# Optimization experiments

Hardware: AMD Instinct MI355X
Metric: run time of the kernel (lower is better)

## Reference

```python
import jax, jax.numpy as jnp
import numpy as np

B, S, D, H = 2, 2048, 4096, 32
Dh = D // H          # 128, rotary_dim == head_dim
BASE = 10000.0       # rope_theta
SCALE = Dh ** -0.5


def setup_inputs() -> dict:
    key = jax.random.key(0)
    k0, k1, k2 = jax.random.split(key, 3)
    w_scale = 0.02
    return {
        "hidden_states": jax.random.normal(k0, (B, S, D), jnp.float32),
        "positions": jnp.broadcast_to(jnp.arange(S, dtype=jnp.int32), (B, S)),
        "Wqkv": jax.random.normal(k1, (D, 3 * D), jnp.float32) * w_scale,
        "bqkv": jnp.zeros((3 * D,), jnp.float32),
        "Wproj": jax.random.normal(k2, (D, D), jnp.float32) * w_scale,
    }


def _apply_rope(x, positions):
    # x: [B, S, H, Dh]; neox-style (rotate-half) RoPE, as in vLLM PagedAttentionWithRoPE
    half = Dh // 2
    inv_freq = 1.0 / (BASE ** (jnp.arange(half, dtype=jnp.float32) / half))
    ang = positions[..., None].astype(jnp.float32) * inv_freq      # [B, S, half]
    cos = jnp.cos(ang)[:, :, None, :]                              # [B, S, 1, half]
    sin = jnp.sin(ang)[:, :, None, :]
    x1, x2 = x[..., :half], x[..., half:]
    return jnp.concatenate([x1 * cos - x2 * sin, x2 * cos + x1 * sin], axis=-1)


def reference(hidden_states, positions, Wqkv, bqkv, Wproj):
    # c_attn: fused QKV projection
    qkv = hidden_states @ Wqkv + bqkv                              # [B, S, 3D]
    q, k, v = jnp.split(qkv, 3, axis=-1)
    q = q.reshape(B, S, H, Dh)
    k = k.reshape(B, S, H, Dh)
    v = v.reshape(B, S, H, Dh)
    # fused RoPE on q and k at the given positions
    q = _apply_rope(q, positions)
    k = _apply_rope(k, positions)
    # causal scaled-dot-product attention (prefill semantics of paged attention)
    scores = jnp.einsum("bqhd,bkhd->bhqk", q, k) * SCALE           # [B, H, S, S]
    causal = jnp.tril(jnp.ones((S, S), dtype=bool))
    scores = jnp.where(causal, scores, jnp.finfo(scores.dtype).min)
    attn = jax.nn.softmax(scores, axis=-1)
    ctx = jnp.einsum("bhqk,bkhd->bqhd", attn, v).reshape(B, S, D)
    # c_proj (no bias)
    return ctx @ Wproj
```

## Files before the change

### kernel.cpp

```cpp
#include <hip/hip_runtime.h>

typedef __attribute__((ext_vector_type(8))) short short8;
typedef __attribute__((ext_vector_type(4))) short short4v;
typedef __attribute__((ext_vector_type(4))) float f32x4;

#define LDS8(base, off) (*(const short8*)((const char*)(base) + (off)))
#define GLOAD_LDS16(gp, lp) __builtin_amdgcn_global_load_lds( \
    (const __attribute__((address_space(1))) unsigned int*)(gp), \
    (__attribute__((address_space(3))) unsigned int*)(lp), 16, 0, 0)
#define SBAR() __builtin_amdgcn_s_barrier()
#define WAIT_LGKM0() do { asm volatile("s_waitcnt lgkmcnt(0)"); __builtin_amdgcn_sched_barrier(0); } while (0)

__device__ __forceinline__ short f2bf(float f) {
    unsigned u = __builtin_bit_cast(unsigned, f);
    unsigned r = (u + 0x7FFFu + ((u >> 16) & 1u)) >> 16;
    return (short)r;
}
__device__ __forceinline__ float bf2f(short s) {
    unsigned u = ((unsigned)(unsigned short)s) << 16;
    return __builtin_bit_cast(float, u);
}

__global__ __launch_bounds__(256) void cvt_f32_bf16(const float* __restrict__ in,
                                                    short* __restrict__ out, int n8) {
    int i = blockIdx.x * 256 + threadIdx.x;
    if (i < n8) {
        const f32x4* p = (const f32x4*)(in + (size_t)i * 8);
        f32x4 a = p[0], bq = p[1];
        short8 o;
        o[0] = f2bf(a[0]); o[1] = f2bf(a[1]); o[2] = f2bf(a[2]); o[3] = f2bf(a[3]);
        o[4] = f2bf(bq[0]); o[5] = f2bf(bq[1]); o[6] = f2bf(bq[2]); o[7] = f2bf(bq[3]);
        *(short8*)(out + (size_t)i * 8) = o;
    }
}

__global__ __launch_bounds__(256) void transpose_cvt(const float* __restrict__ W,
                                                     short* __restrict__ Out, int R, int C) {
    __shared__ float tile[64][33];
    int c0 = blockIdx.x * 64, r0 = blockIdx.y * 32;
    int tid = threadIdx.x;
    int cc4 = (tid & 15) * 4;
#pragma unroll
    for (int it = 0; it < 2; ++it) {
        int rr = (tid >> 4) + it * 16;
        f32x4 v = *(const f32x4*)&W[(size_t)(r0 + rr) * C + c0 + cc4];
#pragma unroll
        for (int i = 0; i < 4; ++i) tile[cc4 + i][rr] = v[i];
    }
    __syncthreads();
    int cc = tid >> 2, r8 = (tid & 3) * 8;
    short8 o;
#pragma unroll
    for (int i = 0; i < 8; ++i) o[i] = f2bf(tile[cc][r8 + i]);
    *(short8*)&Out[(size_t)(c0 + cc) * R + r0 + r8] = o;
}

__global__ __launch_bounds__(256) void rope_table(float* __restrict__ ctab, float* __restrict__ stab) {
    int idx = blockIdx.x * 256 + threadIdx.x;
    int t = idx >> 6, j = idx & 63;
    float inv = expf(-(float)j * (9.210340371976184f / 64.0f));
    float ang = (float)t * inv;
    ctab[idx] = cosf(ang);
    stab[idx] = sinf(ang);
}

__global__ __launch_bounds__(256) void rope_scatter(const short* __restrict__ qkv,
                                                    const int* __restrict__ pos,
                                                    const float* __restrict__ ctab,
                                                    const float* __restrict__ stab,
                                                    short* __restrict__ Q, short* __restrict__ K) {
    int id = blockIdx.x * 256 + threadIdx.x;
    int j = id & 63;
    int h = (id >> 6) & 31;
    int s = (id >> 11) & 2047;
    int b = id >> 22;
    size_t qrow = (size_t)(b * 2048 + s) * 12288 + h * 128;
    float q1 = bf2f(qkv[qrow + j]),        q2 = bf2f(qkv[qrow + 64 + j]);
    float k1 = bf2f(qkv[qrow + 4096 + j]), k2 = bf2f(qkv[qrow + 4160 + j]);
    int p = pos[b * 2048 + s];
    float c = ctab[p * 64 + j], si = stab[p * 64 + j];
    size_t orow = ((size_t)(b * 32 + h) * 2048 + s) * 128;
    Q[orow + j]      = f2bf(q1 * c - q2 * si);
    Q[orow + 64 + j] = f2bf(q2 * c + q1 * si);
    K[orow + j]      = f2bf(k1 * c - k2 * si);
    K[orow + 64 + j] = f2bf(k2 * c + k1 * si);
}

__global__ __launch_bounds__(256) void v_transpose(const short* __restrict__ qkv,
                                                   short* __restrict__ Vt) {
    int bh = blockIdx.z; int b = bh >> 5, h = bh & 31;
    int s0 = blockIdx.x * 64, d0 = blockIdx.y * 64;
    __shared__ short tile[64][65];
    int tid = threadIdx.x;
    int sl = tid >> 3;
    int d8 = (tid & 7) * 8;
#pragma unroll
    for (int it = 0; it < 2; ++it) {
        int s = sl + it * 32;
        short8 v = *(const short8*)&qkv[(size_t)(b * 2048 + s0 + s) * 12288 + 8192 + h * 128 + d0 + d8];
#pragma unroll
        for (int i = 0; i < 8; ++i) tile[s][d8 + i] = v[i];
    }
    __syncthreads();
    int dl = tid >> 3;
    int s8 = (tid & 7) * 8;
#pragma unroll
    for (int it = 0; it < 2; ++it) {
        int d = dl + it * 32;
        short8 o;
#pragma unroll
        for (int i = 0; i < 8; ++i) o[i] = tile[s8 + i][d];
        *(short8*)&Vt[((size_t)bh * 128 + d0 + d) * 2048 + s0 + s8] = o;
    }
}

__global__ __launch_bounds__(512, 2) void gemm256(const short* __restrict__ A,
                                                  const short* __restrict__ Bt,
                                                  const float* __restrict__ bias,
                                                  short* __restrict__ Cbf,
                                                  float* __restrict__ Cf,
                                                  int M, int N, int K, int nN) {
    __shared__ __align__(16) char smem[131072];
    const int tid = threadIdx.x;
    const int l = tid & 63, w = tid >> 6;
    const int m = l & 15, g = l >> 4, m7 = m & 7;
    const int wm = w >> 2, wn = w & 3;

    int cpx = gridDim.x >> 3;
    int wg = (blockIdx.x & 7) * cpx + (blockIdx.x >> 3);
    int gsz = nN << 3;
    int grp = wg / gsz, rem = wg - grp * gsz;
    int bm = (grp << 3) + (rem & 7);
    int bn = rem >> 3;
    int m0 = bm << 8, n0 = bn << 8;

    const int srow = l >> 3;
    const int sgcol = ((l & 7) ^ srow) << 3;

    const int NT = K >> 6;

    const int AbaseR = wm << 14;
    const int BbaseR = 32768 + ((wn >> 1) << 14);
    const int brow0 = (wn & 1) << 6;

    f32x4 acc[8][4];
    const f32x4 fz = {0.f, 0.f, 0.f, 0.f};
#pragma unroll
    for (int i = 0; i < 8; ++i)
#pragma unroll
        for (int j = 0; j < 4; ++j) acc[i][j] = fz;

    auto stage_half = [&](const short* G, int grow0, int kcol, int ldsoff) {
        GLOAD_LDS16(G + (size_t)(grow0 +      w * 8 + srow) * K + kcol + sgcol,
                    smem + ldsoff + w * 1024);
        GLOAD_LDS16(G + (size_t)(grow0 + 64 + w * 8 + srow) * K + kcol + sgcol,
                    smem + ldsoff + 8192 + w * 1024);
    };

    short8 af[2][2], bf[4][2];

#define RD_A(I0)                                                                 \
    _Pragma("unroll")                                                            \
    for (int i2 = 0; i2 < 2; ++i2) {                                             \
        _Pragma("unroll")                                                        \
        for (int kk = 0; kk < 2; ++kk)                                           \
            af[i2][kk] = LDS8(Ab, (((I0) + i2) * 16 + m) * 128 + (((kk * 4 + g) ^ m7) << 4)); \
    }

#define MFMA_IP(IP)                                                              \
    do {                                                                         \
        __builtin_amdgcn_s_setprio(1);                                           \
        _Pragma("unroll")                                                        \
        for (int kk = 0; kk < 2; ++kk) {                                         \
            _Pragma("unroll")                                                    \
            for (int i2 = 0; i2 < 2; ++i2) {                                     \
                _Pragma("unroll")                                                \
                for (int j2 = 0; j2 < 4; ++j2) {                                 \
                    acc[(IP) * 2 + i2][j2] = __builtin_amdgcn_mfma_f32_16x16x32_bf16( \
                        af[i2][kk], bf[j2][kk], acc[(IP) * 2 + i2][j2], 0, 0, 0); \
                }                                                                \
            }                                                                    \
        }                                                                        \
        __builtin_amdgcn_s_setprio(0);                                           \
    } while (0)

#pragma unroll
    for (int t = 0; t < 2; ++t) {
        int sb = t << 16;
        stage_half(A,  m0,       t * 64, sb);
        stage_half(A,  m0 + 128, t * 64, sb + 16384);
        stage_half(Bt, n0,       t * 64, sb + 32768);
        stage_half(Bt, n0 + 128, t * 64, sb + 49152);
    }
    asm volatile("s_waitcnt vmcnt(8)");
    __builtin_amdgcn_sched_barrier(0);
    SBAR();

    for (int kt = 0; kt < NT; ++kt) {
        const int slotb = (kt & 1) << 16;
        const char* Ab = smem + slotb + AbaseR;
        const char* Bb = smem + slotb + BbaseR;
        const bool pf = (kt + 2) < NT;
        const int kc = (kt + 2) << 6;

#pragma unroll
        for (int j = 0; j < 4; ++j) {
#pragma unroll
            for (int kk = 0; kk < 2; ++kk)
                bf[j][kk] = LDS8(Bb, (brow0 + j * 16 + m) * 128 + (((kk * 4 + g) ^ m7) << 4));
        }
        RD_A(0);
        asm volatile("s_waitcnt lgkmcnt(8)");
        SBAR();
        WAIT_LGKM0();
        MFMA_IP(0);
        SBAR();

        RD_A(2);
        if (pf) stage_half(Bt, n0, kc, slotb + 32768);
        SBAR();
        WAIT_LGKM0();
        MFMA_IP(1);
        SBAR();

        RD_A(4);
        if (pf) stage_half(Bt, n0 + 128, kc, slotb + 49152);
        SBAR();
        WAIT_LGKM0();
        MFMA_IP(2);
        SBAR();

        RD_A(6);
        SBAR();
        WAIT_LGKM0();
        MFMA_IP(3);
        if (pf) {
            stage_half(A, m0,       kc, slotb);
            stage_half(A, m0 + 128, kc, slotb + 16384);
        }
        if (kt == NT - 2)     asm volatile("s_waitcnt vmcnt(0)");
        else if (kt < NT - 1) asm volatile("s_waitcnt vmcnt(6)");
        SBAR();
    }
#undef RD_A
#undef MFMA_IP

#pragma unroll
    for (int i = 0; i < 8; ++i) {
#pragma unroll
        for (int j = 0; j < 4; ++j) {
#pragma unroll
            for (int r = 0; r < 4; ++r) {
                int row = m0 + wm * 128 + i * 16 + g * 4 + r;
                int col = n0 + wn * 64 + j * 16 + m;
                float v = acc[i][j][r];
                if (bias) v += bias[col];
                if (Cbf) Cbf[(size_t)row * N + col] = f2bf(v);
                else     Cf[(size_t)row * N + col] = v;
            }
        }
    }
}

__global__ __launch_bounds__(512, 4) void flash_fwd(const short* __restrict__ Q,
                                                    const short* __restrict__ Kt,
                                                    const short* __restrict__ Vt,
                                                    short* __restrict__ ctx) {
    const int S = 2048;
    const float SCALE = 0.08838834764831845f;
    __shared__ __align__(16) char smem[81920];

    int tid = threadIdx.x, l = tid & 63, w = tid >> 6;
    int m = l & 15, g = l >> 4, m7 = m & 7;
    int qg = blockIdx.x, h = blockIdx.y, b = blockIdx.z;
    int bh = b * 32 + h;
    int q0 = qg * 128 + w * 16;

    const short* Qg = Q + ((size_t)bh * S + q0) * 128;
    const short* Kg = Kt + (size_t)bh * S * 128;
    const short* Vg = Vt + (size_t)bh * 128 * S;

    short8 qf[4];
#pragma unroll
    for (int kb = 0; kb < 4; ++kb)
        qf[kb] = *(const short8*)(Qg + m * 128 + kb * 32 + g * 8);

    const f32x4 fz = {0.f, 0.f, 0.f, 0.f};
    f32x4 O[8];
#pragma unroll
    for (int nb = 0; nb < 8; ++nb) O[nb] = fz;
    float Mr[4], Lr[4];
#pragma unroll
    for (int r = 0; r < 4; ++r) { Mr[r] = -__builtin_inff(); Lr[r] = 0.f; }

    const short* Kp[2]; const short* Vp[2]; int KlO[2], VlO[2];
#pragma unroll
    for (int q = 0; q < 2; ++q) {
        int c = w * 2 + q;
        int rowK = c * 4 + (l >> 4);
        Kp[q] = Kg + (size_t)rowK * 128 + (((l & 15) ^ (rowK & 7)) * 8);
        KlO[q] = c * 1024;
        int rowV = c * 8 + (l >> 3);
        Vp[q] = Vg + (size_t)rowV * S + (((l & 7) ^ (rowV & 7)) * 8);
        VlO[q] = c * 1024;
    }

    auto stage = [&](int t, int slot) {
#pragma unroll
        for (int q = 0; q < 2; ++q) {
            GLOAD_LDS16(Kp[q] + (size_t)t * 8192, smem + slot * 16384 + KlO[q]);
            GLOAD_LDS16(Vp[q] + t * 64, smem + 32768 + slot * 16384 + VlO[q]);
        }
    };

    int nkt = 2 * qg + 2;
    stage(0, 0);
    asm volatile("s_waitcnt vmcnt(0)");
    __builtin_amdgcn_sched_barrier(0);
    SBAR();

    for (int kt = 0; kt < nkt; ++kt) {
        if (kt + 1 < nkt) stage(kt + 1, (kt + 1) & 1);
        const char* Kl = smem + (kt & 1) * 16384;
        const char* Vl = smem + 32768 + (kt & 1) * 16384;
        char* Pl = smem + 65536 + w * 2048;
        int k0 = kt * 64;
        if (k0 <= q0 + 15) {
            f32x4 sc[4];
#pragma unroll
            for (int j = 0; j < 4; ++j) sc[j] = fz;
#pragma unroll
            for (int kb = 0; kb < 4; ++kb) {
#pragma unroll
                for (int j = 0; j < 4; ++j) {
                    short8 kf = LDS8(Kl, (j * 16 + m) * 256 + (((kb * 4 + g) ^ m7) << 4));
                    sc[j] = __builtin_amdgcn_mfma_f32_16x16x32_bf16(qf[kb], kf, sc[j], 0, 0, 0);
                }
            }
            bool diag = (k0 + 63 > q0);
#pragma unroll
            for (int r = 0; r < 4; ++r) {
                int qrow = q0 + g * 4 + r;
                float s0 = sc[0][r] * SCALE;
                float s1 = sc[1][r] * SCALE;
                float s2 = sc[2][r] * SCALE;
                float s3 = sc[3][r] * SCALE;
                if (diag) {
                    if (k0 + m > qrow)      s0 = -__builtin_inff();
                    if (k0 + 16 + m > qrow) s1 = -__builtin_inff();
                    if (k0 + 32 + m > qrow) s2 = -__builtin_inff();
                    if (k0 + 48 + m > qrow) s3 = -__builtin_inff();
                }
                float mx = fmaxf(fmaxf(s0, s1), fmaxf(s2, s3));
                mx = fmaxf(mx, __shfl_xor(mx, 1, 64));
                mx = fmaxf(mx, __shfl_xor(mx, 2, 64));
                mx = fmaxf(mx, __shfl_xor(mx, 4, 64));
                mx = fmaxf(mx, __shfl_xor(mx, 8, 64));
                float mnew = fmaxf(Mr[r], mx);
                float alpha = __expf(Mr[r] - mnew);
                float p0 = __expf(s0 - mnew);
                float p1 = __expf(s1 - mnew);
                float p2 = __expf(s2 - mnew);
                float p3 = __expf(s3 - mnew);
                float rs = (p0 + p1) + (p2 + p3);
                rs += __shfl_xor(rs, 1, 64);
                rs += __shfl_xor(rs, 2, 64);
                rs += __shfl_xor(rs, 4, 64);
                rs += __shfl_xor(rs, 8, 64);
                Lr[r] = Lr[r] * alpha + rs;
                Mr[r] = mnew;
#pragma unroll
                for (int nb = 0; nb < 8; ++nb) O[nb][r] *= alpha;
                int pr = g * 4 + r;
                char* pw = Pl + pr * 128;
                float pv[4] = {p0, p1, p2, p3};
#pragma unroll
                for (int j = 0; j < 4; ++j) {
                    int lb = j * 32 + m * 2;
                    int pb = (((lb >> 4) ^ (pr & 7)) << 4) | (lb & 15);
                    *(short*)(pw + pb) = f2bf(pv[j]);
                }
            }
            short8 pf[2];
#pragma unroll
            for (int kh = 0; kh < 2; ++kh)
                pf[kh] = LDS8(Pl, m * 128 + (((kh * 4 + g) ^ m7) << 4));
#pragma unroll
            for (int kh = 0; kh < 2; ++kh) {
#pragma unroll
                for (int nb = 0; nb < 8; ++nb) {
                    int d = nb * 16 + m;
                    short8 vf = LDS8(Vl, d * 128 + (((kh * 4 + g) ^ m7) << 4));
                    O[nb] = __builtin_amdgcn_mfma_f32_16x16x32_bf16(pf[kh], vf, O[nb], 0, 0, 0);
                }
            }
        }
        if (kt + 1 < nkt) {
            asm volatile("s_waitcnt vmcnt(0)");
            __builtin_amdgcn_sched_barrier(0);
            SBAR();
        }
    }
#pragma unroll
    for (int nb = 0; nb < 8; ++nb) {
#pragma unroll
        for (int r = 0; r < 4; ++r) {
            int row = q0 + g * 4 + r;
            float v = O[nb][r] / Lr[r];
            ctx[(size_t)(b * S + row) * 4096 + h * 128 + nb * 16 + m] = f2bf(v);
        }
    }
}

extern "C" void kernel_launch(void* const* d_in, const int* in_sizes, int n_in,
                              void* d_out, int out_size, void* d_ws, size_t ws_size,
                              hipStream_t stream) {
    const float* hidden    = (const float*)d_in[0];
    const int*   positions = (const int*)d_in[1];
    const float* Wqkv      = (const float*)d_in[2];
    const float* bqkv      = (const float*)d_in[3];
    const float* Wproj     = (const float*)d_in[4];
    float* out = (float*)d_out;
    char* ws = (char*)d_ws;

    short* Abf    = (short*)(ws + 0ull);
    short* WqkvT  = (short*)(ws + 33554432ull);
    short* WprojT = (short*)(ws + 134217728ull);
    short* qkv    = (short*)(ws + 167772160ull);
    short* Qr     = (short*)(ws + 268435456ull);
    short* Kr     = (short*)(ws + 301989888ull);
    short* Vt     = (short*)(ws + 335544320ull);
    short* ctx    = (short*)(ws + 369098752ull);
    float* ctab   = (float*)(ws + 402653184ull);
    float* stab   = (float*)(ws + 403177472ull);

    cvt_f32_bf16<<<8192, 256, 0, stream>>>(hidden, Abf, 2097152);
    transpose_cvt<<<dim3(192, 128), 256, 0, stream>>>(Wqkv, WqkvT, 4096, 12288);
    transpose_cvt<<<dim3(64, 128), 256, 0, stream>>>(Wproj, WprojT, 4096, 4096);
    rope_table<<<512, 256, 0, stream>>>(ctab, stab);
    gemm256<<<dim3(768), 512, 0, stream>>>(Abf, WqkvT, bqkv, qkv, nullptr, 4096, 12288, 4096, 48);
    rope_scatter<<<32768, 256, 0, stream>>>(qkv, positions, ctab, stab, Qr, Kr);
    v_transpose<<<dim3(32, 2, 64), 256, 0, stream>>>(qkv, Vt);
    flash_fwd<<<dim3(16, 32, 2), 512, 0, stream>>>(Qr, Kr, Vt, ctx);
    gemm256<<<dim3(256), 512, 0, stream>>>(ctx, WprojT, nullptr, nullptr, out, 4096, 4096, 4096, 16);
}
```

Before: 900.7 us.

## Double-buffer A fragments and drop per-subtile barriers in GEMM main loop

Restructures the GEMM inner loop to read A fragments into two alternating register sets so LDS reads overlap MFMAs, using partial lgkmcnt waits instead of full waits. The three intra-iteration workgroup barriers are removed, and all next-tile global-to-LDS prefetches are issued together after a single barrier per iteration. This reduces synchronization stalls but uses more VGPRs and issues the B prefetch later, which may reduce load/compute overlap.

```diff
diff --git a/kernel.cpp b/kernel.cpp
--- a/kernel.cpp
+++ b/kernel.cpp
@@ -9,7 +9,7 @@
     (const __attribute__((address_space(1))) unsigned int*)(gp), \
     (__attribute__((address_space(3))) unsigned int*)(lp), 16, 0, 0)
 #define SBAR() __builtin_amdgcn_s_barrier()
-#define WAIT_LGKM0() do { asm volatile("s_waitcnt lgkmcnt(0)"); __builtin_amdgcn_sched_barrier(0); } while (0)
+#define SB0() __builtin_amdgcn_sched_barrier(0)
 
 __device__ __forceinline__ short f2bf(float f) {
     unsigned u = __builtin_bit_cast(unsigned, f);
@@ -157,17 +157,17 @@
                     smem + ldsoff + 8192 + w * 1024);
     };
 
-    short8 af[2][2], bf[4][2];
-
-#define RD_A(I0)                                                                 \
+    short8 afX[2][2], afY[2][2], bf[4][2];
+
+#define RD_AF(DST, I0)                                                           \
     _Pragma("unroll")                                                            \
     for (int i2 = 0; i2 < 2; ++i2) {                                             \
         _Pragma("unroll")                                                        \
         for (int kk = 0; kk < 2; ++kk)                                           \
-            af[i2][kk] = LDS8(Ab, (((I0) + i2) * 16 + m) * 128 + (((kk * 4 + g) ^ m7) << 4)); \
-    }
-
-#define MFMA_IP(IP)                                                              \
+            DST[i2][kk] = LDS8(Ab, (((I0) + i2) * 16 + m) * 128 + (((kk * 4 + g) ^ m7) << 4)); \
+    }
+
+#define MFMA_IP(IP, AF)                                                          \
     do {                                                                         \
         __builtin_amdgcn_s_setprio(1);                                           \
         _Pragma("unroll")                                                        \
@@ -177,7 +177,7 @@
                 _Pragma("unroll")                                                \
                 for (int j2 = 0; j2 < 4; ++j2) {                                 \
                     acc[(IP) * 2 + i2][j2] = __builtin_amdgcn_mfma_f32_16x16x32_bf16( \
-                        af[i2][kk], bf[j2][kk], acc[(IP) * 2 + i2][j2], 0, 0, 0); \
+                        AF[i2][kk], bf[j2][kk], acc[(IP) * 2 + i2][j2], 0, 0, 0); \
                 }                                                                \
             }                                                                    \
         }                                                                        \
@@ -193,7 +193,7 @@
         stage_half(Bt, n0 + 128, t * 64, sb + 49152);
     }
     asm volatile("s_waitcnt vmcnt(8)");
-    __builtin_amdgcn_sched_barrier(0);
+    SB0();
     SBAR();
 
     for (int kt = 0; kt < NT; ++kt) {
@@ -209,40 +209,41 @@
             for (int kk = 0; kk < 2; ++kk)
                 bf[j][kk] = LDS8(Bb, (brow0 + j * 16 + m) * 128 + (((kk * 4 + g) ^ m7) << 4));
         }
-        RD_A(0);
-        asm volatile("s_waitcnt lgkmcnt(8)");
+        RD_AF(afX, 0);
+        RD_AF(afY, 2);
+        SB0();
+        asm volatile("s_waitcnt lgkmcnt(4)");
+        SB0();
+        MFMA_IP(0, afX);
+        RD_AF(afX, 4);
+        SB0();
+        asm volatile("s_waitcnt lgkmcnt(4)");
+        SB0();
+        MFMA_IP(1, afY);
+        RD_AF(afY, 6);
+        SB0();
+        asm volatile("s_waitcnt lgkmcnt(4)");
+        SB0();
+        MFMA_IP(2, afX);
+        asm volatile("s_waitcnt lgkmcnt(0)");
+        SB0();
+        MFMA_IP(3, afY);
+
         SBAR();
-        WAIT_LGKM0();
-        MFMA_IP(0);
-        SBAR();
-
-        RD_A(2);
-        if (pf) stage_half(Bt, n0, kc, slotb + 32768);
-        SBAR();
-        WAIT_LGKM0();
-        MFMA_IP(1);
-        SBAR();
-
-        RD_A(4);
-        if (pf) stage_half(Bt, n0 + 128, kc, slotb + 49152);
-        SBAR();
-        WAIT_LGKM0();
-        MFMA_IP(2);
-        SBAR();
-
-        RD_A(6);
-        SBAR();
-        WAIT_LGKM0();
-        MFMA_IP(3);
         if (pf) {
-            stage_half(A, m0,       kc, slotb);
-            stage_half(A, m0 + 128, kc, slotb + 16384);
-        }
-        if (kt == NT - 2)     asm volatile("s_waitcnt vmcnt(0)");
-        else if (kt < NT - 1) asm volatile("s_waitcnt vmcnt(6)");
-        SBAR();
-    }
-#undef RD_A
+            stage_half(A,  m0,       kc, slotb);
+            stage_half(A,  m0 + 128, kc, slotb + 16384);
+            stage_half(Bt, n0,       kc, slotb + 32768);
+            stage_half(Bt, n0 + 128, kc, slotb + 49152);
+        }
+        if (kt + 1 < NT) {
+            if (pf) asm volatile("s_waitcnt vmcnt(8)");
+            else    asm volatile("s_waitcnt vmcnt(0)");
+            SB0();
+            SBAR();
+        }
+    }
+#undef RD_AF
 #undef MFMA_IP
 
 #pragma unroll
@@ -316,7 +317,7 @@
     int nkt = 2 * qg + 2;
     stage(0, 0);
     asm volatile("s_waitcnt vmcnt(0)");
-    __builtin_amdgcn_sched_barrier(0);
+    SB0();
     SBAR();
 
     for (int kt = 0; kt < nkt; ++kt) {
@@ -397,7 +398,7 @@
         }
         if (kt + 1 < nkt) {
             asm volatile("s_waitcnt vmcnt(0)");
-            __builtin_amdgcn_sched_barrier(0);
+            SB0();
             SBAR();
         }
     }
```

After: 937.2 us. 4.1% more time.
